# Kernel tuning notes

Measured on AMD Instinct MI355X. Metric: run time of the kernel, lower is better.

## Reference

```python
import jax, jax.numpy as jnp
import numpy as np

IN_FEATURES = 4096
OUT_FEATURES = 11008
BATCH, SEQ = 4, 2048


def setup_inputs() -> dict:
    key = jax.random.key(0)
    k1, k2, k3 = jax.random.split(key, 3)
    x = jax.random.normal(k1, (BATCH, SEQ, IN_FEATURES), dtype=jnp.float32)
    # int8-valued weights stored as int32 (values in [-128, 127])
    weight_int8 = jax.random.randint(k2, (OUT_FEATURES, IN_FEATURES), -128, 128, dtype=jnp.int32)
    # per-output-channel positive scales, typical magnitude ~ max|w|/127
    scale = jax.random.uniform(k3, (OUT_FEATURES,), dtype=jnp.float32, minval=1e-4, maxval=0.05)
    return {"x": x, "weight_int8": weight_int8, "scale": scale}


def reference(x, weight_int8, scale):
    # Dequantize: per-channel symmetric, weight[o, i] = int8[o, i] * scale[o]
    weight = weight_int8.astype(x.dtype) * scale.astype(x.dtype)[:, None]
    # F.linear: x @ weight.T  -> [B, S, out_features]
    return jnp.einsum("bsi,oi->bso", x, weight)
```

## Files before the change

### kernel.cpp

```cpp
#include <hip/hip_runtime.h>
#include <hip/hip_bf16.h>


#define M_DIM 8192
#define N_DIM 11008
#define K_DIM 4096

#define BM 256
#define BN 256
#define BK 128

using f32x4 = __attribute__((ext_vector_type(4))) float;
using i32x4 = __attribute__((ext_vector_type(4))) int;
using s16x4 = __attribute__((ext_vector_type(4))) short;
using s16x8 = __attribute__((ext_vector_type(8))) short;

typedef __attribute__((address_space(3))) void lds_void_t;
typedef __attribute__((address_space(1))) const void gbl_void_t;

__device__ __forceinline__ short cvt_bf16(float f) {
    union { float f; unsigned u; } v; v.f = f;
    unsigned r = v.u + 0x7fffu + ((v.u >> 16) & 1u);
    return (short)(r >> 16);
}

__global__ __launch_bounds__(256) void quant_x(const float* __restrict__ X,
                                               signed char* __restrict__ Q,
                                               float* __restrict__ sx) {
    const int row = blockIdx.x;
    const int tid = threadIdx.x;
    const f32x4* xr = (const f32x4*)(X + (size_t)row * K_DIM);

    f32x4 v[4];
    float m = 0.f;
    #pragma unroll
    for (int i = 0; i < 4; ++i) {
        v[i] = xr[tid * 4 + i];
        #pragma unroll
        for (int j = 0; j < 4; ++j) m = fmaxf(m, fabsf(v[i][j]));
    }
    #pragma unroll
    for (int off = 32; off; off >>= 1) m = fmaxf(m, __shfl_xor(m, off));
    __shared__ float wmax[4];
    if ((tid & 63) == 0) wmax[tid >> 6] = m;
    __syncthreads();
    m = fmaxf(fmaxf(wmax[0], wmax[1]), fmaxf(wmax[2], wmax[3]));

    const float inv = (m > 0.f) ? 127.0f / m : 0.f;
    i32x4 o;
    #pragma unroll
    for (int i = 0; i < 4; ++i) {
        int b0 = __float2int_rn(v[i][0] * inv) & 255;
        int b1 = __float2int_rn(v[i][1] * inv) & 255;
        int b2 = __float2int_rn(v[i][2] * inv) & 255;
        int b3 = __float2int_rn(v[i][3] * inv) & 255;
        o[i] = b0 | (b1 << 8) | (b2 << 16) | (b3 << 24);
    }
    ((i32x4*)(Q + (size_t)row * K_DIM))[tid] = o;
    if (tid == 0) sx[row] = (m > 0.f) ? m * (1.0f / 127.0f) : 0.f;
}

__global__ __launch_bounds__(256) void convert_w(const int* __restrict__ W,
                                                 signed char* __restrict__ Q, int n16) {
    int i = blockIdx.x * blockDim.x + threadIdx.x;
    const int stride = gridDim.x * blockDim.x;
    for (; i < n16; i += stride) {
        i32x4 o;
        #pragma unroll
        for (int j = 0; j < 4; ++j) {
            i32x4 v = ((const i32x4*)W)[i * 4 + j];
            o[j] = (v[0] & 255) | ((v[1] & 255) << 8) | ((v[2] & 255) << 16) | (v[3] << 24);
        }
        ((i32x4*)Q)[i] = o;
    }
}

#define SBAR __builtin_amdgcn_s_barrier()
#define LGKM(n) do { asm volatile("s_waitcnt lgkmcnt(" #n ")" ::: "memory"); \
                     __builtin_amdgcn_sched_barrier(0); } while (0)
#define WAIT_VM(n) do { asm volatile("s_waitcnt vmcnt(" #n ")" ::: "memory"); \
                        __builtin_amdgcn_sched_barrier(0); } while (0)

#define STAGE(bufi, opi, srcp, T) do {                                             \
    signed char* _d = &lds[bufi][opi][0];                                          \
    const size_t _toff = (size_t)((T) & 31) * 128;                                 \
    _Pragma("unroll")                                                              \
    for (int _i = 0; _i < 4; ++_i)                                                 \
        __builtin_amdgcn_global_load_lds(                                          \
            (gbl_void_t*)((srcp) + (size_t)_i * 64 * K_DIM + _toff),               \
            (lds_void_t*)(_d + (_i * 512 + tid) * 16), 16, 0, 0);                  \
} while (0)

#define READ_A(dst, bufi, qm) do {                                                 \
    const signed char* _s = &lds[bufi][0][0];                                      \
    _Pragma("unroll")                                                              \
    for (int _m = 0; _m < 4; ++_m)                                                 \
        _Pragma("unroll")                                                          \
        for (int _k = 0; _k < 2; ++_k)                                             \
            dst[_m][_k] = *(const i32x4*)(_s                                       \
                + (size_t)((mi * 128 + (qm) * 64 + _m * 16 + fr) * 128)            \
                + ((((_k << 2) | fq) ^ fr7) << 4));                                \
} while (0)

#define READ_B(dst, bufi, qn) do {                                                 \
    const signed char* _s = &lds[bufi][1][0];                                      \
    _Pragma("unroll")                                                              \
    for (int _n = 0; _n < 2; ++_n)                                                 \
        _Pragma("unroll")                                                          \
        for (int _k = 0; _k < 2; ++_k)                                             \
            dst[_n][_k] = *(const i32x4*)(_s                                       \
                + (size_t)((ni * 64 + (qn) * 32 + _n * 16 + fr) * 128)             \
                + ((((_k << 2) | fq) ^ fr7) << 4));                                \
} while (0)

#define MFMA_Q(qm, qn, aset, bset) do {                                            \
    __builtin_amdgcn_s_setprio(1);                                                 \
    _Pragma("unroll")                                                              \
    for (int _m = 0; _m < 4; ++_m)                                                 \
        _Pragma("unroll")                                                          \
        for (int _n = 0; _n < 2; ++_n)                                             \
            _Pragma("unroll")                                                      \
            for (int _k = 0; _k < 2; ++_k)                                         \
                acc[(qm) * 4 + _m][(qn) * 2 + _n] =                                \
                    __builtin_amdgcn_mfma_i32_16x16x64_i8(                         \
                        aset[_m][_k], bset[_n][_k],                                \
                        acc[(qm) * 4 + _m][(qn) * 2 + _n], 0, 0, 0);               \
    __builtin_amdgcn_s_setprio(0);                                                 \
} while (0)

#define HALF_ITER(BUF, OBUF, BQ0, BQ1, T) do {                                     \
    READ_B(BQ1, BUF, 1);                                                           \
    LGKM(4);                                                                       \
    MFMA_Q(0, 0, a0, BQ0);                                                         \
    SBAR;                                                                          \
    READ_A(a1, BUF, 1);                                                            \
    LGKM(8);                                                                       \
    MFMA_Q(0, 1, a0, BQ1);                                                         \
    SBAR;                                                                          \
    STAGE(BUF, 1, Bsrc, (T) + 2);                                                  \
    LGKM(0);                                                                       \
    MFMA_Q(1, 1, a1, BQ1);                                                         \
    WAIT_VM(4);                                                                    \
    SBAR;                                                                          \
    STAGE(BUF, 0, Asrc, (T) + 2);                                                  \
    READ_A(a0, OBUF, 0);                                                           \
    READ_B(BQ1, OBUF, 0);                                                          \
    LGKM(12);                                                                      \
    MFMA_Q(1, 0, a1, BQ0);                                                         \
    SBAR;                                                                          \
} while (0)

__global__ __launch_bounds__(512, 2) void gemm_i8(
    const signed char* __restrict__ A,
    const signed char* __restrict__ B,
    const float* __restrict__ sx,
    const float* __restrict__ scale,
    float*       __restrict__ C)
{
    __shared__ __align__(16) signed char lds[2][2][256 * 128];

    const int tid  = threadIdx.x;
    const int lane = tid & 63;
    const int fr   = lane & 15;
    const int fq   = lane >> 4;
    const int fr7  = fr & 7;
    const int wave = tid >> 6;
    const int mi   = wave >> 2;
    const int ni   = wave & 3;

    const int bid = blockIdx.x;
    const int xcd = bid & 7;
    const int idx = bid >> 3;
    const int bm  = xcd * 4 + (idx & 3);
    const int bn  = idx >> 2;

    const int jl   = (tid & 7) ^ ((tid >> 3) & 7);
    const int soff = (tid >> 3) * K_DIM + jl * 16;
    const signed char* Asrc = A + (size_t)bm * BM * K_DIM + soff;
    const signed char* Bsrc = B + (size_t)bn * BN * K_DIM + soff;

    i32x4 acc[8][4] = {};
    i32x4 a0[4][2], a1[4][2], b_a[2][2], b_b[2][2];

    STAGE(0, 1, Bsrc, 0);
    STAGE(0, 0, Asrc, 0);
    STAGE(1, 1, Bsrc, 1);
    STAGE(1, 0, Asrc, 1);
    WAIT_VM(8);
    SBAR;
    READ_A(a0, 0, 0);
    READ_B(b_a, 0, 0);

    for (int it = 0; it < 16; ++it) {
        const int t0 = 2 * it;
        HALF_ITER(0, 1, b_a, b_b, t0);
        HALF_ITER(1, 0, b_b, b_a, t0 + 1);
    }

    const int row0 = bm * BM + mi * 128 + fq * 4;
    const int col0 = bn * BN + ni * 64 + fr;
    float s4[4];
    #pragma unroll
    for (int jn = 0; jn < 4; ++jn) s4[jn] = scale[col0 + jn * 16];
    #pragma unroll
    for (int i = 0; i < 8; ++i) {
        float sxv[4];
        #pragma unroll
        for (int jj = 0; jj < 4; ++jj) sxv[jj] = sx[row0 + i * 16 + jj];
        #pragma unroll
        for (int jn = 0; jn < 4; ++jn)
            #pragma unroll
            for (int jj = 0; jj < 4; ++jj)
                __builtin_nontemporal_store(
                    (float)acc[i][jn][jj] * sxv[jj] * s4[jn],
                    &C[(size_t)(row0 + i * 16 + jj) * N_DIM + col0 + jn * 16]);
    }
}

#define FBM 128
#define FBN 128
#define FBK 32
#define LDK 40
__global__ __launch_bounds__(256) void int8_linear_fused(
    const float* __restrict__ A, const int* __restrict__ W,
    const float* __restrict__ scale, float* __restrict__ C)
{
    __shared__ short As[FBM][LDK];
    __shared__ short Bs[FBN][LDK];
    const int tid = threadIdx.x;
    const int bid = blockIdx.x;
    const int g   = bid / (8 * 86);
    const int rem = bid % (8 * 86);
    const int bm  = g * 8 + (rem & 7);
    const int bn  = rem >> 3;
    const int srow = tid >> 3;
    const int skq  = tid & 7;
    const float* Ab = A + (size_t)(bm * FBM + srow) * K_DIM + skq * 4;
    const int*   Wb = W + (size_t)(bn * FBN + srow) * K_DIM + skq * 4;
    const int lane = tid & 63, wave = tid >> 6;
    const int wm = (wave >> 1) * 64, wn = (wave & 1) * 64;
    const int fr = lane & 15, fq = lane >> 4;
    f32x4 acc[4][4] = {};
    f32x4 areg[4]; i32x4 breg[4];
    #pragma unroll
    for (int i = 0; i < 4; ++i) {
        areg[i] = *(const f32x4*)(Ab + (size_t)(i * 32) * K_DIM);
        breg[i] = *(const i32x4*)(Wb + (size_t)(i * 32) * K_DIM);
    }
    const int NT = K_DIM / FBK;
    for (int kt = 0; kt < NT; ++kt) {
        __syncthreads();
        #pragma unroll
        for (int i = 0; i < 4; ++i) {
            s16x4 av, bv;
            #pragma unroll
            for (int j = 0; j < 4; ++j) {
                av[j] = cvt_bf16(areg[i][j]);
                bv[j] = cvt_bf16((float)breg[i][j]);
            }
            *(s16x4*)&As[srow + i * 32][skq * 4] = av;
            *(s16x4*)&Bs[srow + i * 32][skq * 4] = bv;
        }
        __syncthreads();
        if (kt + 1 < NT) {
            const int k0 = (kt + 1) * FBK;
            #pragma unroll
            for (int i = 0; i < 4; ++i) {
                areg[i] = *(const f32x4*)(Ab + (size_t)(i * 32) * K_DIM + k0);
                breg[i] = *(const i32x4*)(Wb + (size_t)(i * 32) * K_DIM + k0);
            }
        }
        s16x8 af[4], bf[4];
        #pragma unroll
        for (int m = 0; m < 4; ++m) af[m] = *(const s16x8*)&As[wm + m * 16 + fr][fq * 8];
        #pragma unroll
        for (int n = 0; n < 4; ++n) bf[n] = *(const s16x8*)&Bs[wn + n * 16 + fr][fq * 8];
        #pragma unroll
        for (int m = 0; m < 4; ++m)
            #pragma unroll
            for (int n = 0; n < 4; ++n)
                acc[m][n] = __builtin_amdgcn_mfma_f32_16x16x32_bf16(af[m], bf[n], acc[m][n], 0, 0, 0);
    }
    #pragma unroll
    for (int n = 0; n < 4; ++n) {
        const int gn = bn * FBN + wn + n * 16 + fr;
        const float s = scale[gn];
        #pragma unroll
        for (int m = 0; m < 4; ++m) {
            const int gm0 = bm * FBM + wm + m * 16 + fq * 4;
            #pragma unroll
            for (int j = 0; j < 4; ++j)
                C[(size_t)(gm0 + j) * N_DIM + gn] = acc[m][n][j] * s;
        }
    }
}

extern "C" void kernel_launch(void* const* d_in, const int* in_sizes, int n_in,
                              void* d_out, int out_size, void* d_ws, size_t ws_size,
                              hipStream_t stream) {
    const float* x  = (const float*)d_in[0];
    const int*   w  = (const int*)d_in[1];
    const float* sc = (const float*)d_in[2];
    float* out = (float*)d_out;

    const size_t w_bytes  = (size_t)N_DIM * K_DIM;
    const size_t x_bytes  = (size_t)M_DIM * K_DIM;
    const size_t sx_bytes = (size_t)M_DIM * sizeof(float);
    const size_t need = w_bytes + x_bytes + sx_bytes;

    if (ws_size >= need) {
        signed char* qw = (signed char*)d_ws;
        signed char* qx = qw + w_bytes;
        float* sx = (float*)(qx + x_bytes);
        convert_w<<<dim3(2048), dim3(256), 0, stream>>>(w, qw, (int)(w_bytes / 16));
        quant_x<<<dim3(M_DIM), dim3(256), 0, stream>>>(x, qx, sx);
        const int nblocks = (M_DIM / BM) * (N_DIM / BN);
        gemm_i8<<<dim3(nblocks), dim3(512), 0, stream>>>(qx, qw, sx, sc, out);
    } else {
        const int nblocks = (M_DIM / FBM) * (N_DIM / FBN);
        int8_linear_fused<<<dim3(nblocks), dim3(256), 0, stream>>>(x, w, sc, out);
    }
}
```

Baseline: 425.2 us.

## Switch int8 GEMM to 32x32x32 MFMA tiles with matching LDS fragment reads

Replaces the 16x16x64 int8 MFMA tiling with 32x32x32 int8 MFMAs. Fragment loads from LDS, the accumulator layout and the epilogue row/column mapping change to fit the 32x32 output layout. It also hoists the A-fragment read ahead of the first MFMA quarter and removes one barrier. The larger MFMA shape gives more compute per LDS fragment read and may raise matrix-core throughput. The risks are a different LDS bank-conflict pattern under the same swizzle and different register pressure.

Result: slower. 476.0 us (+12.0%).

```diff
diff --git a/kernel.cpp b/kernel.cpp
--- a/kernel.cpp
+++ b/kernel.cpp
@@ -10,10 +10,11 @@
 #define BN 256
 #define BK 128
 
-using f32x4 = __attribute__((ext_vector_type(4))) float;
-using i32x4 = __attribute__((ext_vector_type(4))) int;
-using s16x4 = __attribute__((ext_vector_type(4))) short;
-using s16x8 = __attribute__((ext_vector_type(8))) short;
+using f32x4  = __attribute__((ext_vector_type(4))) float;
+using i32x4  = __attribute__((ext_vector_type(4))) int;
+using i32x16 = __attribute__((ext_vector_type(16))) int;
+using s16x4  = __attribute__((ext_vector_type(4))) short;
+using s16x8  = __attribute__((ext_vector_type(8))) short;
 
 typedef __attribute__((address_space(3))) void lds_void_t;
 typedef __attribute__((address_space(1))) const void gbl_void_t;
@@ -94,46 +95,39 @@
 #define READ_A(dst, bufi, qm) do {                                                 \
     const signed char* _s = &lds[bufi][0][0];                                      \
     _Pragma("unroll")                                                              \
-    for (int _m = 0; _m < 4; ++_m)                                                 \
+    for (int _f = 0; _f < 2; ++_f)                                                 \
         _Pragma("unroll")                                                          \
-        for (int _k = 0; _k < 2; ++_k)                                             \
-            dst[_m][_k] = *(const i32x4*)(_s                                       \
-                + (size_t)((mi * 128 + (qm) * 64 + _m * 16 + fr) * 128)            \
-                + ((((_k << 2) | fq) ^ fr7) << 4));                                \
+        for (int _k = 0; _k < 4; ++_k)                                             \
+            dst[_f][_k] = *(const i32x4*)(_s                                       \
+                + (size_t)((mi * 128 + (qm) * 64 + _f * 32 + l31) * 128)           \
+                + ((((_k << 1) | l5) ^ l7) << 4));                                 \
 } while (0)
 
 #define READ_B(dst, bufi, qn) do {                                                 \
     const signed char* _s = &lds[bufi][1][0];                                      \
     _Pragma("unroll")                                                              \
-    for (int _n = 0; _n < 2; ++_n)                                                 \
-        _Pragma("unroll")                                                          \
-        for (int _k = 0; _k < 2; ++_k)                                             \
-            dst[_n][_k] = *(const i32x4*)(_s                                       \
-                + (size_t)((ni * 64 + (qn) * 32 + _n * 16 + fr) * 128)             \
-                + ((((_k << 2) | fq) ^ fr7) << 4));                                \
+    for (int _k = 0; _k < 4; ++_k)                                                 \
+        dst[_k] = *(const i32x4*)(_s                                               \
+            + (size_t)((ni * 64 + (qn) * 32 + l31) * 128)                          \
+            + ((((_k << 1) | l5) ^ l7) << 4));                                     \
 } while (0)
 
 #define MFMA_Q(qm, qn, aset, bset) do {                                            \
     __builtin_amdgcn_s_setprio(1);                                                 \
     _Pragma("unroll")                                                              \
-    for (int _m = 0; _m < 4; ++_m)                                                 \
+    for (int _f = 0; _f < 2; ++_f)                                                 \
         _Pragma("unroll")                                                          \
-        for (int _n = 0; _n < 2; ++_n)                                             \
-            _Pragma("unroll")                                                      \
-            for (int _k = 0; _k < 2; ++_k)                                         \
-                acc[(qm) * 4 + _m][(qn) * 2 + _n] =                                \
-                    __builtin_amdgcn_mfma_i32_16x16x64_i8(                         \
-                        aset[_m][_k], bset[_n][_k],                                \
-                        acc[(qm) * 4 + _m][(qn) * 2 + _n], 0, 0, 0);               \
+        for (int _k = 0; _k < 4; ++_k)                                             \
+            acc[(qm) * 2 + _f][qn] = __builtin_amdgcn_mfma_i32_32x32x32_i8(        \
+                aset[_f][_k], bset[_k], acc[(qm) * 2 + _f][qn], 0, 0, 0);          \
     __builtin_amdgcn_s_setprio(0);                                                 \
 } while (0)
 
 #define HALF_ITER(BUF, OBUF, BQ0, BQ1, T) do {                                     \
     READ_B(BQ1, BUF, 1);                                                           \
-    LGKM(4);                                                                       \
+    READ_A(a1, BUF, 1);                                                            \
+    LGKM(12);                                                                      \
     MFMA_Q(0, 0, a0, BQ0);                                                         \
-    SBAR;                                                                          \
-    READ_A(a1, BUF, 1);                                                            \
     LGKM(8);                                                                       \
     MFMA_Q(0, 1, a0, BQ1);                                                         \
     SBAR;                                                                          \
@@ -161,9 +155,9 @@
 
     const int tid  = threadIdx.x;
     const int lane = tid & 63;
-    const int fr   = lane & 15;
-    const int fq   = lane >> 4;
-    const int fr7  = fr & 7;
+    const int l31  = lane & 31;
+    const int l5   = lane >> 5;
+    const int l7   = l31 & 7;
     const int wave = tid >> 6;
     const int mi   = wave >> 2;
     const int ni   = wave & 3;
@@ -179,8 +173,9 @@
     const signed char* Asrc = A + (size_t)bm * BM * K_DIM + soff;
     const signed char* Bsrc = B + (size_t)bn * BN * K_DIM + soff;
 
-    i32x4 acc[8][4] = {};
-    i32x4 a0[4][2], a1[4][2], b_a[2][2], b_b[2][2];
+    i32x16 acc[4][2] = {};
+    i32x4  a0[2][4], a1[2][4];
+    i32x4  b_a[4], b_b[4];
 
     STAGE(0, 1, Bsrc, 0);
     STAGE(0, 0, Asrc, 0);
@@ -197,23 +192,27 @@
         HALF_ITER(1, 0, b_b, b_a, t0 + 1);
     }
 
-    const int row0 = bm * BM + mi * 128 + fq * 4;
-    const int col0 = bn * BN + ni * 64 + fr;
-    float s4[4];
-    #pragma unroll
-    for (int jn = 0; jn < 4; ++jn) s4[jn] = scale[col0 + jn * 16];
-    #pragma unroll
-    for (int i = 0; i < 8; ++i) {
-        float sxv[4];
-        #pragma unroll
-        for (int jj = 0; jj < 4; ++jj) sxv[jj] = sx[row0 + i * 16 + jj];
-        #pragma unroll
-        for (int jn = 0; jn < 4; ++jn)
-            #pragma unroll
-            for (int jj = 0; jj < 4; ++jj)
+    const int row0 = bm * BM + mi * 128 + l5 * 4;
+    const int col0 = bn * BN + ni * 64 + l31;
+    #pragma unroll
+    for (int am = 0; am < 4; ++am) {
+        const int rb = row0 + am * 32;
+        float sxv[16];
+        #pragma unroll
+        for (int reg = 0; reg < 16; ++reg)
+            sxv[reg] = sx[rb + (reg & 3) + 8 * (reg >> 2)];
+        #pragma unroll
+        for (int an = 0; an < 2; ++an) {
+            const int cb = col0 + an * 32;
+            const float sc_v = scale[cb];
+            #pragma unroll
+            for (int reg = 0; reg < 16; ++reg) {
+                const int r = rb + (reg & 3) + 8 * (reg >> 2);
                 __builtin_nontemporal_store(
-                    (float)acc[i][jn][jj] * sxv[jj] * s4[jn],
-                    &C[(size_t)(row0 + i * 16 + jj) * N_DIM + col0 + jn * 16]);
+                    (float)acc[am][an][reg] * sxv[reg] * sc_v,
+                    &C[(size_t)r * N_DIM + cb]);
+            }
+        }
     }
 }
 
```

## Reschedule int8 GEMM main loop to issue LDS reads earlier and drop a barrier

Applied to the files above, without the earlier changes.

Restructures the half-iteration schedule of the int8 MFMA GEMM. A and B fragment reads for the second half are issued together up front, the next B fragment goes into a separate register set (three B buffers instead of two), and one block barrier per half-iteration is removed. Global-load waits change to a full vmcnt(0) drain before staging. The epilogue store loop is also reordered to go row by row. The aim is more overlap of LDS reads with MFMA and less barrier stalling. The costs are extra register pressure under the occupancy-2 launch bound and a possible loss of load latency hiding from the full vmcnt wait. Removing the barrier also risks an LDS race.

Result: no change. 418.4 us (-1.6%).

```diff
diff --git a/kernel.cpp b/kernel.cpp
--- a/kernel.cpp
+++ b/kernel.cpp
@@ -10,10 +10,10 @@
 #define BN 256
 #define BK 128
 
-using f32x4 = __attribute__((ext_vector_type(4))) float;
-using i32x4 = __attribute__((ext_vector_type(4))) int;
-using s16x4 = __attribute__((ext_vector_type(4))) short;
-using s16x8 = __attribute__((ext_vector_type(8))) short;
+using f32x4  = __attribute__((ext_vector_type(4))) float;
+using i32x4  = __attribute__((ext_vector_type(4))) int;
+using s16x4  = __attribute__((ext_vector_type(4))) short;
+using s16x8  = __attribute__((ext_vector_type(8))) short;
 
 typedef __attribute__((address_space(3))) void lds_void_t;
 typedef __attribute__((address_space(1))) const void gbl_void_t;
@@ -128,26 +128,27 @@
     __builtin_amdgcn_s_setprio(0);                                                 \
 } while (0)
 
-#define HALF_ITER(BUF, OBUF, BQ0, BQ1, T) do {                                     \
-    READ_B(BQ1, BUF, 1);                                                           \
-    LGKM(4);                                                                       \
-    MFMA_Q(0, 0, a0, BQ0);                                                         \
+#define HALF_ITER(BUF, OBUF, B0, B0N, T) do {                                      \
+                                                    \
+    READ_B(b1, BUF, 1);                                                            \
+    READ_A(a1, BUF, 1);                                                            \
+    LGKM(12);                                                                      \
+    MFMA_Q(0, 0, a0, B0);                                                          \
     SBAR;                                                                          \
-    READ_A(a1, BUF, 1);                                                            \
+              \
+    MFMA_Q(0, 1, a0, b1);                                                          \
+    WAIT_VM(0);                                                                    \
+    SBAR;                                                                          \
+                    \
+    STAGE(BUF, 1, Bsrc, (T) + 2);                                                  \
+    READ_A(a0, OBUF, 0);                                                           \
     LGKM(8);                                                                       \
-    MFMA_Q(0, 1, a0, BQ1);                                                         \
+    MFMA_Q(1, 1, a1, b1);                                                          \
     SBAR;                                                                          \
-    STAGE(BUF, 1, Bsrc, (T) + 2);                                                  \
-    LGKM(0);                                                                       \
-    MFMA_Q(1, 1, a1, BQ1);                                                         \
-    WAIT_VM(4);                                                                    \
-    SBAR;                                                                          \
+        \
     STAGE(BUF, 0, Asrc, (T) + 2);                                                  \
-    READ_A(a0, OBUF, 0);                                                           \
-    READ_B(BQ1, OBUF, 0);                                                          \
-    LGKM(12);                                                                      \
-    MFMA_Q(1, 0, a1, BQ0);                                                         \
-    SBAR;                                                                          \
+    READ_B(B0N, OBUF, 0);                                                          \
+    MFMA_Q(1, 0, a1, B0);                                                          \
 } while (0)
 
 __global__ __launch_bounds__(512, 2) void gemm_i8(
@@ -180,7 +181,8 @@
     const signed char* Bsrc = B + (size_t)bn * BN * K_DIM + soff;
 
     i32x4 acc[8][4] = {};
-    i32x4 a0[4][2], a1[4][2], b_a[2][2], b_b[2][2];
+    i32x4 a0[4][2], a1[4][2];
+    i32x4 b0e[2][2], b0o[2][2], b1[2][2];
 
     STAGE(0, 1, Bsrc, 0);
     STAGE(0, 0, Asrc, 0);
@@ -189,12 +191,11 @@
     WAIT_VM(8);
     SBAR;
     READ_A(a0, 0, 0);
-    READ_B(b_a, 0, 0);
-
+    READ_B(b0e, 0, 0);
     for (int it = 0; it < 16; ++it) {
         const int t0 = 2 * it;
-        HALF_ITER(0, 1, b_a, b_b, t0);
-        HALF_ITER(1, 0, b_b, b_a, t0 + 1);
+        HALF_ITER(0, 1, b0e, b0o, t0);
+        HALF_ITER(1, 0, b0o, b0e, t0 + 1);
     }
 
     const int row0 = bm * BM + mi * 128 + fq * 4;
@@ -204,16 +205,16 @@
     for (int jn = 0; jn < 4; ++jn) s4[jn] = scale[col0 + jn * 16];
     #pragma unroll
     for (int i = 0; i < 8; ++i) {
-        float sxv[4];
-        #pragma unroll
-        for (int jj = 0; jj < 4; ++jj) sxv[jj] = sx[row0 + i * 16 + jj];
-        #pragma unroll
-        for (int jn = 0; jn < 4; ++jn)
-            #pragma unroll
-            for (int jj = 0; jj < 4; ++jj)
+        #pragma unroll
+        for (int jj = 0; jj < 4; ++jj) {
+            const int r = row0 + i * 16 + jj;
+            const float sxv = sx[r];
+            #pragma unroll
+            for (int jn = 0; jn < 4; ++jn)
                 __builtin_nontemporal_store(
-                    (float)acc[i][jn][jj] * sxv[jj] * s4[jn],
-                    &C[(size_t)(row0 + i * 16 + jj) * N_DIM + col0 + jn * 16]);
+                    (float)acc[i][jn][jj] * sxv * s4[jn],
+                    &C[(size_t)r * N_DIM + col0 + jn * 16]);
+        }
     }
 }
 
```
